# Kernel optimization log

Measured on AMD Instinct MI355X. Metric: run time of the kernel, lower is better.

## Reference

```python
import jax, jax.numpy as jnp
import numpy as np

D_MODEL = 1024
NUM_HEADS = 16


def setup_inputs() -> dict:
    key = jax.random.key(0)
    ks = jax.random.split(key, 5)
    B, S, D = 2, 2048, D_MODEL
    scale = 1.0 / np.sqrt(D)
    return {
        "x": jax.random.normal(ks[0], (B, S, D), dtype=jnp.float32),
        "q_proj_weight": jax.random.normal(ks[1], (D, D), dtype=jnp.float32) * scale,
        "k_proj_weight": jax.random.normal(ks[2], (D, D), dtype=jnp.float32) * scale,
        "v_proj_weight": jax.random.normal(ks[3], (D, D), dtype=jnp.float32) * scale,
        "o_proj_weight": jax.random.normal(ks[4], (D, D), dtype=jnp.float32) * scale,
    }


def _attn(x, qw, kw, vw, ow, num_heads):
    B, S, D = x.shape
    d_k = D // num_heads
    q = x @ qw.T  # [B,S,D]
    k = x @ kw.T
    v = x @ vw.T
    # split heads: [B, H, S, d_k]
    q = q.reshape(B, S, num_heads, d_k).transpose(0, 2, 1, 3)
    k = k.reshape(B, S, num_heads, d_k).transpose(0, 2, 1, 3)
    v = v.reshape(B, S, num_heads, d_k).transpose(0, 2, 1, 3)
    scores = jnp.einsum('bhqd,bhkd->bhqk', q, k) / jnp.sqrt(jnp.asarray(d_k, x.dtype))
    causal = jnp.tril(jnp.ones((S, S), dtype=bool))  # [S,S]
    scores = jnp.where(causal[None, None], scores, jnp.asarray(-jnp.inf, x.dtype))
    attn = jax.nn.softmax(scores, axis=-1)
    out = jnp.einsum('bhqk,bhkd->bhqd', attn, v)  # [B,H,S,d_k]
    out = out.transpose(0, 2, 1, 3).reshape(B, S, D)
    return out @ ow.T


def reference(x, q_proj_weight, k_proj_weight, v_proj_weight, o_proj_weight):
    return _attn(x, q_proj_weight, k_proj_weight, v_proj_weight, o_proj_weight, NUM_HEADS)
```

## Files before the change

kernel.cpp:

```cpp
#include <hip/hip_runtime.h>

typedef __attribute__((ext_vector_type(8))) short short8;
typedef __attribute__((ext_vector_type(4))) float f32x4;

#define MFMA(a,b,c) __builtin_amdgcn_mfma_f32_16x16x32_bf16((a),(b),(c),0,0,0)

#define B_  2
#define S_  2048
#define D_  1024
#define H_  16
#define DK  64
#define KDIM 1024

typedef unsigned int u32;
typedef __attribute__((address_space(1))) const u32 gu32;
typedef __attribute__((address_space(3))) u32 lu32;

__device__ __forceinline__ void gll16(const unsigned short* g, unsigned short* l){
  __builtin_amdgcn_global_load_lds((gu32*)g, (lu32*)l, 16, 0, 0);
}

__device__ __forceinline__ unsigned short f2bf(float f){
  unsigned int u = __float_as_uint(f);
  u += 0x7fffu + ((u >> 16) & 1u);
  return (unsigned short)(u >> 16);
}

__device__ __forceinline__ u32 pkbf(float lo, float hi){
  u32 a = __float_as_uint(lo) + 0x8000u;
  u32 b = __float_as_uint(hi) + 0x8000u;
  return __builtin_amdgcn_perm(b, a, 0x07060302u);
}

__global__ void cvt_all(const float* __restrict__ x,  const float* __restrict__ qw,
                        const float* __restrict__ kw, const float* __restrict__ vw,
                        const float* __restrict__ ow,
                        unsigned short* __restrict__ xb,  unsigned short* __restrict__ wqb,
                        unsigned short* __restrict__ wkb, unsigned short* __restrict__ wvb,
                        unsigned short* __restrict__ wob,
                        int n4x, int n4w){
  int i = blockIdx.x * 256 + threadIdx.x;
  const float* src; unsigned short* dst; int n4;
  switch (blockIdx.y) {
    case 0:  src = x;  dst = xb;  n4 = n4x; break;
    case 1:  src = qw; dst = wqb; n4 = n4w; break;
    case 2:  src = kw; dst = wkb; n4 = n4w; break;
    case 3:  src = vw; dst = wvb; n4 = n4w; break;
    default: src = ow; dst = wob; n4 = n4w; break;
  }
  if (i >= n4) return;
  float4 f = reinterpret_cast<const float4*>(src)[i];
  ushort4 u;
  u.x = f2bf(f.x); u.y = f2bf(f.y); u.z = f2bf(f.z); u.w = f2bf(f.w);
  reinterpret_cast<ushort4*>(dst)[i] = u;
}

struct Frags { short8 a0[4], a1[4], b0[2], b1[2]; };

__global__ __launch_bounds__(256) void gemm_qkv(
    const unsigned short* __restrict__ X,
    const unsigned short* __restrict__ Wq,
    const unsigned short* __restrict__ Wk,
    const unsigned short* __restrict__ Wv,
    unsigned short* __restrict__ Qo,
    unsigned short* __restrict__ Ko,
    unsigned short* __restrict__ Vo)
{
  const int z = blockIdx.z;
  const unsigned short* __restrict__ W = (z == 0) ? Wq : (z == 1) ? Wk : Wv;
  const int n0 = blockIdx.x * 64;
  const int m0 = blockIdx.y * 128;

  __shared__ unsigned short As[2][128 * 64];
  __shared__ unsigned short Bs[2][64 * 64];

  const int tid  = threadIdx.x;
  const int wid  = tid >> 6, lane = tid & 63;
  const int wm   = (wid >> 1) * 64, wn = (wid & 1) * 32;
  const int lr   = lane & 15, c = lane >> 4;
  const int sw   = lr & 7;
  const int pc0  = (c ^ sw) * 8;
  const int pc1  = ((c ^ 4) ^ sw) * 8;

  const int srow = lane >> 3;
  const int scol = ((lane & 7) ^ srow) * 8;
  const unsigned short* gA = X + (size_t)(m0 + wid * 32 + srow) * KDIM + scol;
  const unsigned short* gB = W + (size_t)(n0 + wid * 16 + srow) * KDIM + scol;

  auto stage = [&](int buf, int k0) {
    unsigned short* la = &As[buf][(wid * 32) * 64];
    unsigned short* lb = &Bs[buf][(wid * 16) * 64];
#pragma unroll
    for (int i = 0; i < 4; i++) gll16(gA + (size_t)(i * 8) * KDIM + k0, la + i * 512);
#pragma unroll
    for (int i = 0; i < 2; i++) gll16(gB + (size_t)(i * 8) * KDIM + k0, lb + i * 512);
  };

  auto ldfr = [&](int buf, Frags& f) {
    const unsigned short* AS = As[buf];
    const unsigned short* BS = Bs[buf];
#pragma unroll
    for (int i = 0; i < 4; i++) {
      f.a0[i] = *(const short8*)&AS[(wm + i * 16 + lr) * 64 + pc0];
      f.a1[i] = *(const short8*)&AS[(wm + i * 16 + lr) * 64 + pc1];
    }
#pragma unroll
    for (int j = 0; j < 2; j++) {
      f.b0[j] = *(const short8*)&BS[(wn + j * 16 + lr) * 64 + pc0];
      f.b1[j] = *(const short8*)&BS[(wn + j * 16 + lr) * 64 + pc1];
    }
  };

  f32x4 acc[4][2];
  const f32x4 z4 = {0.f, 0.f, 0.f, 0.f};
  for (int i = 0; i < 4; i++)
    for (int j = 0; j < 2; j++) acc[i][j] = z4;

  auto mfmas = [&](const Frags& f) {
    if (z == 2) {
#pragma unroll
      for (int i = 0; i < 4; i++)
#pragma unroll
        for (int j = 0; j < 2; j++) {
          acc[i][j] = MFMA(f.b0[j], f.a0[i], acc[i][j]);
          acc[i][j] = MFMA(f.b1[j], f.a1[i], acc[i][j]);
        }
    } else {
#pragma unroll
      for (int i = 0; i < 4; i++)
#pragma unroll
        for (int j = 0; j < 2; j++) {
          acc[i][j] = MFMA(f.a0[i], f.b0[j], acc[i][j]);
          acc[i][j] = MFMA(f.a1[i], f.b1[j], acc[i][j]);
        }
    }
  };

  stage(0, 0);
  stage(1, 64);

  Frags f;
  const int NT = KDIM / 64;
  for (int t = 0; t < NT - 2; ++t) {
    const int buf = t & 1;
    asm volatile("s_waitcnt vmcnt(6)" ::: "memory");
    __builtin_amdgcn_s_barrier();
    asm volatile("" ::: "memory");
    ldfr(buf, f);
    asm volatile("s_waitcnt lgkmcnt(0)" ::: "memory");
    __builtin_amdgcn_sched_barrier(0);
    __builtin_amdgcn_s_barrier();
    asm volatile("" ::: "memory");
    stage(buf, (t + 2) * 64);
    __builtin_amdgcn_sched_barrier(0);
    mfmas(f);
  }
  asm volatile("s_waitcnt vmcnt(6)" ::: "memory");
  __builtin_amdgcn_s_barrier();
  asm volatile("" ::: "memory");
  ldfr((NT - 2) & 1, f);
  mfmas(f);
  asm volatile("s_waitcnt vmcnt(0)" ::: "memory");
  __builtin_amdgcn_s_barrier();
  asm volatile("" ::: "memory");
  ldfr((NT - 1) & 1, f);
  mfmas(f);

  const int rbase = (lane >> 4) * 4;
  if (z == 2) {
    for (int i = 0; i < 4; i++)
      for (int j = 0; j < 2; j++)
        for (int r = 0; r < 4; r++) {
          int dfull = n0 + wn + j * 16 + rbase + r;
          int sfull = m0 + wm + i * 16 + lr;
          int h = dfull >> 6, d = dfull & 63;
          int bb = sfull >> 11, s = sfull & 2047;
          Vo[(((bb * H_ + h) * DK) + d) * S_ + s] = f2bf(acc[i][j][r]);
        }
  } else {
    for (int i = 0; i < 4; i++)
      for (int j = 0; j < 2; j++)
        for (int r = 0; r < 4; r++) {
          int m = m0 + wm + i * 16 + rbase + r;
          int n = n0 + wn + j * 16 + lr;
          float v = acc[i][j][r];
          int bb = m >> 11, s = m & 2047, h = n >> 6, d = n & 63;
          if (z == 0) {
            v *= 0.18033688f;
            Qo[(((bb * H_ + h) * S_) + s) * DK + d] = f2bf(v);
          } else {
            Ko[(((bb * H_ + h) * S_) + s) * DK + d] = f2bf(v);
          }
        }
  }
}

__global__ __launch_bounds__(512, 4) void attn(
    const unsigned short* __restrict__ Q,
    const unsigned short* __restrict__ K,
    const unsigned short* __restrict__ V,
    unsigned short* __restrict__ O)
{
  const int h = blockIdx.y, b = blockIdx.z;
  const int qt = b ? (15 - blockIdx.x) : blockIdx.x;

  const unsigned short* __restrict__ Qh = Q + (size_t)((b * H_ + h) * S_) * DK;
  const unsigned short* __restrict__ Kh = K + (size_t)((b * H_ + h) * S_) * DK;
  const unsigned short* __restrict__ Vh = V + (size_t)((b * H_ + h) * DK) * S_;

  __shared__ unsigned short Ks0[64 * 64];
  __shared__ unsigned short Ks1[64 * 64];
  __shared__ unsigned short Vs0[64 * 64];
  __shared__ unsigned short Vs1[64 * 64];
  __shared__ unsigned short Ps[8][16][72];

  const int tid = threadIdx.x, wid = tid >> 6, lane = tid & 63;
  const int lr = lane & 15;
  const int row4 = (lane >> 4) * 4;
  const int q0 = qt * 128;
  const int qcol = q0 + wid * 16 + lr;
  const int qwmin = q0 + wid * 16;
  const int qwmax = qwmin + 15;
  const int lk = (lane >> 4) * 8;

  const int pc0 = (((lane >> 4) + lr) & 7) * 8;
  const int pc1 = (((lane >> 4) + 4 + lr) & 7) * 8;

  const int sr8 = lane >> 3;
  const int sc8 = lane & 7;
  const int sg  = (sc8 - sr8) & 7;
  const int stRow = wid * 8 + sr8;
  const unsigned short* gK = Kh + (size_t)stRow * DK + sg * 8;
  const unsigned short* gV = Vh + (size_t)stRow * S_ + sg * 8;
  unsigned short* lK0 = &Ks0[wid * 8 * 64];
  unsigned short* lK1 = &Ks1[wid * 8 * 64];
  unsigned short* lV0 = &Vs0[wid * 8 * 64];
  unsigned short* lV1 = &Vs1[wid * 8 * 64];

  const short ONE = (short)0x3F80;
  const short8 ones = {ONE, ONE, ONE, ONE, ONE, ONE, ONE, ONE};

  short8 qf[2];
  qf[0] = *(const short8*)&Qh[(q0 + wid * 16 + lr) * DK + lk];
  qf[1] = *(const short8*)&Qh[(q0 + wid * 16 + lr) * DK + 32 + lk];

  const f32x4 z4 = {0.f, 0.f, 0.f, 0.f};
  f32x4 o[4];
  for (int i = 0; i < 4; i++) o[i] = z4;
  f32x4 rs = z4;

  auto tile = [&](int k0, const unsigned short* KS, const unsigned short* VS){
    if (k0 > qwmax) return;
    f32x4 sc[4];
    for (int nt = 0; nt < 4; nt++) {
      short8 kb0 = *(const short8*)&KS[(nt * 16 + lr) * 64 + pc0];
      short8 kb1 = *(const short8*)&KS[(nt * 16 + lr) * 64 + pc1];
      f32x4 s = MFMA(kb0, qf[0], z4);
      sc[nt] = MFMA(kb1, qf[1], s);
    }
    if (k0 + 63 > qwmin) {
      for (int nt = 0; nt < 4; nt++) {
        int kg = k0 + nt * 16 + row4;
        for (int r = 0; r < 4; r++)
          if (kg + r > qcol) sc[nt][r] = -INFINITY;
      }
    }
    for (int nt = 0; nt < 4; nt++) {
      float p0 = __builtin_amdgcn_exp2f(sc[nt][0]);
      float p1 = __builtin_amdgcn_exp2f(sc[nt][1]);
      float p2 = __builtin_amdgcn_exp2f(sc[nt][2]);
      float p3 = __builtin_amdgcn_exp2f(sc[nt][3]);
      uint2 pk;
      pk.x = pkbf(p0, p1);
      pk.y = pkbf(p2, p3);
      *(uint2*)&Ps[wid][lr][nt * 16 + row4] = pk;
    }
    short8 pf0 = *(const short8*)&Ps[wid][lr][lk];
    short8 pf1 = *(const short8*)&Ps[wid][lr][32 + lk];
    rs = MFMA(ones, pf0, rs);
    rs = MFMA(ones, pf1, rs);
    for (int dt = 0; dt < 4; dt++) {
      short8 vb0 = *(const short8*)&VS[(dt * 16 + lr) * 64 + pc0];
      short8 vb1 = *(const short8*)&VS[(dt * 16 + lr) * 64 + pc1];
      o[dt] = MFMA(vb0, pf0, o[dt]);
      o[dt] = MFMA(vb1, pf1, o[dt]);
    }
  };

  const int kt_end = 2 * qt + 2;

  gll16(gK, lK0);
  gll16(gV, lV0);

  for (int kt = 0; kt < kt_end; kt += 2) {
    const int k0 = kt * 64;
    __syncthreads();
    {
      gll16(gK + (size_t)(k0 + 64) * DK, lK1);
      gll16(gV + (k0 + 64),              lV1);
    }
    tile(k0, Ks0, Vs0);
    __syncthreads();
    if (kt + 2 < kt_end) {
      gll16(gK + (size_t)(k0 + 128) * DK, lK0);
      gll16(gV + (k0 + 128),              lV0);
    }
    tile(k0 + 64, Ks1, Vs1);
  }

  const float inv = 1.0f / rs[0];

  const int srow = q0 + wid * 16 + lr;
  for (int dt = 0; dt < 4; dt++) {
    uint2 pk;
    pk.x = pkbf(o[dt][0] * inv, o[dt][1] * inv);
    pk.y = pkbf(o[dt][2] * inv, o[dt][3] * inv);
    *(uint2*)&O[(size_t)(b * S_ + srow) * D_ + h * DK + dt * 16 + row4] = pk;
  }
}

__global__ __launch_bounds__(256) void gemm_oproj(
    const unsigned short* __restrict__ A,
    const unsigned short* __restrict__ W,
    float* __restrict__ out)
{
  const int n0 = blockIdx.x * 64;
  const int m0 = blockIdx.y * 128;

  __shared__ unsigned short As[2][128 * 64];
  __shared__ unsigned short Bs[2][64 * 64];

  const int tid  = threadIdx.x;
  const int wid  = tid >> 6, lane = tid & 63;
  const int wm   = (wid >> 1) * 64, wn = (wid & 1) * 32;
  const int lr   = lane & 15, c = lane >> 4;
  const int sw   = lr & 7;
  const int pc0  = (c ^ sw) * 8;
  const int pc1  = ((c ^ 4) ^ sw) * 8;

  const int srow = lane >> 3;
  const int scol = ((lane & 7) ^ srow) * 8;
  const unsigned short* gA = A + (size_t)(m0 + wid * 32 + srow) * KDIM + scol;
  const unsigned short* gB = W + (size_t)(n0 + wid * 16 + srow) * KDIM + scol;

  auto stage = [&](int buf, int k0) {
    unsigned short* la = &As[buf][(wid * 32) * 64];
    unsigned short* lb = &Bs[buf][(wid * 16) * 64];
#pragma unroll
    for (int i = 0; i < 4; i++) gll16(gA + (size_t)(i * 8) * KDIM + k0, la + i * 512);
#pragma unroll
    for (int i = 0; i < 2; i++) gll16(gB + (size_t)(i * 8) * KDIM + k0, lb + i * 512);
  };

  auto ldfr = [&](int buf, Frags& f) {
    const unsigned short* AS = As[buf];
    const unsigned short* BS = Bs[buf];
#pragma unroll
    for (int i = 0; i < 4; i++) {
      f.a0[i] = *(const short8*)&AS[(wm + i * 16 + lr) * 64 + pc0];
      f.a1[i] = *(const short8*)&AS[(wm + i * 16 + lr) * 64 + pc1];
    }
#pragma unroll
    for (int j = 0; j < 2; j++) {
      f.b0[j] = *(const short8*)&BS[(wn + j * 16 + lr) * 64 + pc0];
      f.b1[j] = *(const short8*)&BS[(wn + j * 16 + lr) * 64 + pc1];
    }
  };

  f32x4 acc[4][2];
  const f32x4 z4 = {0.f, 0.f, 0.f, 0.f};
  for (int i = 0; i < 4; i++)
    for (int j = 0; j < 2; j++) acc[i][j] = z4;

  auto mfmas = [&](const Frags& f) {
#pragma unroll
    for (int i = 0; i < 4; i++)
#pragma unroll
      for (int j = 0; j < 2; j++) {
        acc[i][j] = MFMA(f.a0[i], f.b0[j], acc[i][j]);
        acc[i][j] = MFMA(f.a1[i], f.b1[j], acc[i][j]);
      }
  };

  stage(0, 0);
  stage(1, 64);

  Frags f;
  const int NT = KDIM / 64;
  for (int t = 0; t < NT - 2; ++t) {
    const int buf = t & 1;
    asm volatile("s_waitcnt vmcnt(6)" ::: "memory");
    __builtin_amdgcn_s_barrier();
    asm volatile("" ::: "memory");
    ldfr(buf, f);
    asm volatile("s_waitcnt lgkmcnt(0)" ::: "memory");
    __builtin_amdgcn_sched_barrier(0);
    __builtin_amdgcn_s_barrier();
    asm volatile("" ::: "memory");
    stage(buf, (t + 2) * 64);
    __builtin_amdgcn_sched_barrier(0);
    mfmas(f);
  }
  asm volatile("s_waitcnt vmcnt(6)" ::: "memory");
  __builtin_amdgcn_s_barrier();
  asm volatile("" ::: "memory");
  ldfr((NT - 2) & 1, f);
  mfmas(f);
  asm volatile("s_waitcnt vmcnt(0)" ::: "memory");
  __builtin_amdgcn_s_barrier();
  asm volatile("" ::: "memory");
  ldfr((NT - 1) & 1, f);
  mfmas(f);

  const int rbase = (lane >> 4) * 4;
  for (int i = 0; i < 4; i++)
    for (int j = 0; j < 2; j++)
      for (int r = 0; r < 4; r++) {
        int m = m0 + wm + i * 16 + rbase + r;
        int n = n0 + wn + j * 16 + lr;
        out[(size_t)m * D_ + n] = acc[i][j][r];
      }
}

extern "C" void kernel_launch(void* const* d_in, const int* in_sizes, int n_in,
                              void* d_out, int out_size, void* d_ws, size_t ws_size,
                              hipStream_t stream) {
  const float* x  = (const float*)d_in[0];
  const float* qw = (const float*)d_in[1];
  const float* kw = (const float*)d_in[2];
  const float* vw = (const float*)d_in[3];
  const float* ow = (const float*)d_in[4];
  float* out = (float*)d_out;

  char* ws = (char*)d_ws;
  size_t off = 0;
  auto alloc = [&](size_t bytes) -> void* {
    void* p = ws + off;
    off += (bytes + 255) & ~(size_t)255;
    return p;
  };
  const size_t XN = (size_t)B_ * S_ * D_;
  const size_t WN = (size_t)D_ * D_;
  unsigned short* xb  = (unsigned short*)alloc(XN * 2);
  unsigned short* wqb = (unsigned short*)alloc(WN * 2);
  unsigned short* wkb = (unsigned short*)alloc(WN * 2);
  unsigned short* wvb = (unsigned short*)alloc(WN * 2);
  unsigned short* wob = (unsigned short*)alloc(WN * 2);
  unsigned short* Qb  = (unsigned short*)alloc(XN * 2);
  unsigned short* Kb  = (unsigned short*)alloc(XN * 2);
  unsigned short* Vb  = (unsigned short*)alloc(XN * 2);
  unsigned short* Ob  = (unsigned short*)alloc(XN * 2);

  cvt_all<<<dim3((XN / 4 + 255) / 256, 5), dim3(256), 0, stream>>>(
      x, qw, kw, vw, ow, xb, wqb, wkb, wvb, wob, (int)(XN / 4), (int)(WN / 4));

  gemm_qkv<<<dim3(D_ / 64, (B_ * S_) / 128, 3), dim3(256), 0, stream>>>(
      xb, wqb, wkb, wvb, Qb, Kb, Vb);

  attn<<<dim3(S_ / 128, H_, B_), dim3(512), 0, stream>>>(Qb, Kb, Vb, Ob);

  gemm_oproj<<<dim3(D_ / 64, (B_ * S_) / 128), dim3(256), 0, stream>>>(Ob, wob, out);
}
```

Baseline: 162.8 us.

## Fuse Q/K/V projections into one GEMM block sharing the X tile

Measured after the change: 152.6 us. -6.3%, faster.

```diff
diff --git a/kernel.cpp b/kernel.cpp
--- a/kernel.cpp
+++ b/kernel.cpp
@@ -55,9 +55,9 @@
   reinterpret_cast<ushort4*>(dst)[i] = u;
 }
 
-struct Frags { short8 a0[4], a1[4], b0[2], b1[2]; };
-
-__global__ __launch_bounds__(256) void gemm_qkv(
+struct FragsQKV { short8 a0[4], a1[4], b0[3][2], b1[3][2]; };
+
+__global__ __launch_bounds__(256, 2) void gemm_qkv(
     const unsigned short* __restrict__ X,
     const unsigned short* __restrict__ Wq,
     const unsigned short* __restrict__ Wk,
@@ -66,13 +66,11 @@
     unsigned short* __restrict__ Ko,
     unsigned short* __restrict__ Vo)
 {
-  const int z = blockIdx.z;
-  const unsigned short* __restrict__ W = (z == 0) ? Wq : (z == 1) ? Wk : Wv;
   const int n0 = blockIdx.x * 64;
   const int m0 = blockIdx.y * 128;
 
   __shared__ unsigned short As[2][128 * 64];
-  __shared__ unsigned short Bs[2][64 * 64];
+  __shared__ unsigned short Bs[2][3][64 * 64];
 
   const int tid  = threadIdx.x;
   const int wid  = tid >> 6, lane = tid & 63;
@@ -84,7 +82,278 @@
 
   const int srow = lane >> 3;
   const int scol = ((lane & 7) ^ srow) * 8;
-  const unsigned short* gA = X + (size_t)(m0 + wid * 32 + srow) * KDIM + scol;
+  const unsigned short* gA  = X  + (size_t)(m0 + wid * 32 + srow) * KDIM + scol;
+  const unsigned short* gBq = Wq + (size_t)(n0 + wid * 16 + srow) * KDIM + scol;
+  const unsigned short* gBk = Wk + (size_t)(n0 + wid * 16 + srow) * KDIM + scol;
+  const unsigned short* gBv = Wv + (size_t)(n0 + wid * 16 + srow) * KDIM + scol;
+
+  auto stage = [&](int buf, int k0) {
+    unsigned short* la  = &As[buf][(wid * 32) * 64];
+    unsigned short* lbq = &Bs[buf][0][(wid * 16) * 64];
+    unsigned short* lbk = &Bs[buf][1][(wid * 16) * 64];
+    unsigned short* lbv = &Bs[buf][2][(wid * 16) * 64];
+#pragma unroll
+    for (int i = 0; i < 4; i++) gll16(gA + (size_t)(i * 8) * KDIM + k0, la + i * 512);
+#pragma unroll
+    for (int i = 0; i < 2; i++) gll16(gBq + (size_t)(i * 8) * KDIM + k0, lbq + i * 512);
+#pragma unroll
+    for (int i = 0; i < 2; i++) gll16(gBk + (size_t)(i * 8) * KDIM + k0, lbk + i * 512);
+#pragma unroll
+    for (int i = 0; i < 2; i++) gll16(gBv + (size_t)(i * 8) * KDIM + k0, lbv + i * 512);
+  };
+
+  auto ldfr = [&](int buf, FragsQKV& f) {
+    const unsigned short* AS = As[buf];
+#pragma unroll
+    for (int i = 0; i < 4; i++) {
+      f.a0[i] = *(const short8*)&AS[(wm + i * 16 + lr) * 64 + pc0];
+      f.a1[i] = *(const short8*)&AS[(wm + i * 16 + lr) * 64 + pc1];
+    }
+#pragma unroll
+    for (int z = 0; z < 3; z++) {
+      const unsigned short* BS = Bs[buf][z];
+#pragma unroll
+      for (int j = 0; j < 2; j++) {
+        f.b0[z][j] = *(const short8*)&BS[(wn + j * 16 + lr) * 64 + pc0];
+        f.b1[z][j] = *(const short8*)&BS[(wn + j * 16 + lr) * 64 + pc1];
+      }
+    }
+  };
+
+  f32x4 acc[3][4][2];
+  const f32x4 z4 = {0.f, 0.f, 0.f, 0.f};
+#pragma unroll
+  for (int z = 0; z < 3; z++)
+    for (int i = 0; i < 4; i++)
+      for (int j = 0; j < 2; j++) acc[z][i][j] = z4;
+
+  auto mfmas = [&](const FragsQKV& f) {
+#pragma unroll
+    for (int z = 0; z < 3; z++) {
+      if (z == 2) {
+#pragma unroll
+        for (int i = 0; i < 4; i++)
+#pragma unroll
+          for (int j = 0; j < 2; j++) {
+            acc[z][i][j] = MFMA(f.b0[z][j], f.a0[i], acc[z][i][j]);
+            acc[z][i][j] = MFMA(f.b1[z][j], f.a1[i], acc[z][i][j]);
+          }
+      } else {
+#pragma unroll
+        for (int i = 0; i < 4; i++)
+#pragma unroll
+          for (int j = 0; j < 2; j++) {
+            acc[z][i][j] = MFMA(f.a0[i], f.b0[z][j], acc[z][i][j]);
+            acc[z][i][j] = MFMA(f.a1[i], f.b1[z][j], acc[z][i][j]);
+          }
+      }
+    }
+  };
+
+  stage(0, 0);
+  stage(1, 64);
+
+  FragsQKV f;
+  const int NT = KDIM / 64;
+  for (int t = 0; t < NT - 2; ++t) {
+    const int buf = t & 1;
+    asm volatile("s_waitcnt vmcnt(10)" ::: "memory");
+    __builtin_amdgcn_s_barrier();
+    asm volatile("" ::: "memory");
+    ldfr(buf, f);
+    asm volatile("s_waitcnt lgkmcnt(0)" ::: "memory");
+    __builtin_amdgcn_sched_barrier(0);
+    __builtin_amdgcn_s_barrier();
+    asm volatile("" ::: "memory");
+    stage(buf, (t + 2) * 64);
+    __builtin_amdgcn_sched_barrier(0);
+    mfmas(f);
+  }
+  asm volatile("s_waitcnt vmcnt(10)" ::: "memory");
+  __builtin_amdgcn_s_barrier();
+  asm volatile("" ::: "memory");
+  ldfr((NT - 2) & 1, f);
+  mfmas(f);
+  asm volatile("s_waitcnt vmcnt(0)" ::: "memory");
+  __builtin_amdgcn_s_barrier();
+  asm volatile("" ::: "memory");
+  ldfr((NT - 1) & 1, f);
+  mfmas(f);
+
+  const int rbase = (lane >> 4) * 4;
+  for (int i = 0; i < 4; i++)
+    for (int j = 0; j < 2; j++)
+      for (int r = 0; r < 4; r++) {
+        int m = m0 + wm + i * 16 + rbase + r;
+        int n = n0 + wn + j * 16 + lr;
+        int bb = m >> 11, s = m & 2047, h = n >> 6, d = n & 63;
+        float vq = acc[0][i][j][r] * 0.18033688f;
+        Qo[(((bb * H_ + h) * S_) + s) * DK + d] = f2bf(vq);
+        Ko[(((bb * H_ + h) * S_) + s) * DK + d] = f2bf(acc[1][i][j][r]);
+      }
+  for (int i = 0; i < 4; i++)
+    for (int j = 0; j < 2; j++)
+      for (int r = 0; r < 4; r++) {
+        int dfull = n0 + wn + j * 16 + rbase + r;
+        int sfull = m0 + wm + i * 16 + lr;
+        int h = dfull >> 6, d = dfull & 63;
+        int bb = sfull >> 11, s = sfull & 2047;
+        Vo[(((bb * H_ + h) * DK) + d) * S_ + s] = f2bf(acc[2][i][j][r]);
+      }
+}
+
+__global__ __launch_bounds__(512, 4) void attn(
+    const unsigned short* __restrict__ Q,
+    const unsigned short* __restrict__ K,
+    const unsigned short* __restrict__ V,
+    unsigned short* __restrict__ O)
+{
+  const int h = blockIdx.y, b = blockIdx.z;
+  const int qt = b ? (15 - blockIdx.x) : blockIdx.x;
+
+  const unsigned short* __restrict__ Qh = Q + (size_t)((b * H_ + h) * S_) * DK;
+  const unsigned short* __restrict__ Kh = K + (size_t)((b * H_ + h) * S_) * DK;
+  const unsigned short* __restrict__ Vh = V + (size_t)((b * H_ + h) * DK) * S_;
+
+  __shared__ unsigned short Ks0[64 * 64];
+  __shared__ unsigned short Ks1[64 * 64];
+  __shared__ unsigned short Vs0[64 * 64];
+  __shared__ unsigned short Vs1[64 * 64];
+  __shared__ unsigned short Ps[8][16][72];
+
+  const int tid = threadIdx.x, wid = tid >> 6, lane = tid & 63;
+  const int lr = lane & 15;
+  const int row4 = (lane >> 4) * 4;
+  const int q0 = qt * 128;
+  const int qcol = q0 + wid * 16 + lr;
+  const int qwmin = q0 + wid * 16;
+  const int qwmax = qwmin + 15;
+  const int lk = (lane >> 4) * 8;
+
+  const int pc0 = (((lane >> 4) + lr) & 7) * 8;
+  const int pc1 = (((lane >> 4) + 4 + lr) & 7) * 8;
+
+  const int sr8 = lane >> 3;
+  const int sc8 = lane & 7;
+  const int sg  = (sc8 - sr8) & 7;
+  const int stRow = wid * 8 + sr8;
+  const unsigned short* gK = Kh + (size_t)stRow * DK + sg * 8;
+  const unsigned short* gV = Vh + (size_t)stRow * S_ + sg * 8;
+  unsigned short* lK0 = &Ks0[wid * 8 * 64];
+  unsigned short* lK1 = &Ks1[wid * 8 * 64];
+  unsigned short* lV0 = &Vs0[wid * 8 * 64];
+  unsigned short* lV1 = &Vs1[wid * 8 * 64];
+
+  const short ONE = (short)0x3F80;
+  const short8 ones = {ONE, ONE, ONE, ONE, ONE, ONE, ONE, ONE};
+
+  short8 qf[2];
+  qf[0] = *(const short8*)&Qh[(q0 + wid * 16 + lr) * DK + lk];
+  qf[1] = *(const short8*)&Qh[(q0 + wid * 16 + lr) * DK + 32 + lk];
+
+  const f32x4 z4 = {0.f, 0.f, 0.f, 0.f};
+  f32x4 o[4];
+  for (int i = 0; i < 4; i++) o[i] = z4;
+  f32x4 rs = z4;
+
+  auto tile = [&](int k0, const unsigned short* KS, const unsigned short* VS){
+    if (k0 > qwmax) return;
+    f32x4 sc[4];
+    __builtin_amdgcn_s_setprio(1);
+    for (int nt = 0; nt < 4; nt++) {
+      short8 kb0 = *(const short8*)&KS[(nt * 16 + lr) * 64 + pc0];
+      short8 kb1 = *(const short8*)&KS[(nt * 16 + lr) * 64 + pc1];
+      f32x4 s = MFMA(kb0, qf[0], z4);
+      sc[nt] = MFMA(kb1, qf[1], s);
+    }
+    __builtin_amdgcn_s_setprio(0);
+    if (k0 + 63 > qwmin) {
+      for (int nt = 0; nt < 4; nt++) {
+        int kg = k0 + nt * 16 + row4;
+        for (int r = 0; r < 4; r++)
+          if (kg + r > qcol) sc[nt][r] = -INFINITY;
+      }
+    }
+    for (int nt = 0; nt < 4; nt++) {
+      float p0 = __builtin_amdgcn_exp2f(sc[nt][0]);
+      float p1 = __builtin_amdgcn_exp2f(sc[nt][1]);
+      float p2 = __builtin_amdgcn_exp2f(sc[nt][2]);
+      float p3 = __builtin_amdgcn_exp2f(sc[nt][3]);
+      uint2 pk;
+      pk.x = pkbf(p0, p1);
+      pk.y = pkbf(p2, p3);
+      *(uint2*)&Ps[wid][lr][nt * 16 + row4] = pk;
+    }
+    short8 pf0 = *(const short8*)&Ps[wid][lr][lk];
+    short8 pf1 = *(const short8*)&Ps[wid][lr][32 + lk];
+    __builtin_amdgcn_s_setprio(1);
+    rs = MFMA(ones, pf0, rs);
+    rs = MFMA(ones, pf1, rs);
+    for (int dt = 0; dt < 4; dt++) {
+      short8 vb0 = *(const short8*)&VS[(dt * 16 + lr) * 64 + pc0];
+      short8 vb1 = *(const short8*)&VS[(dt * 16 + lr) * 64 + pc1];
+      o[dt] = MFMA(vb0, pf0, o[dt]);
+      o[dt] = MFMA(vb1, pf1, o[dt]);
+    }
+    __builtin_amdgcn_s_setprio(0);
+  };
+
+  const int kt_end = 2 * qt + 2;
+
+  gll16(gK, lK0);
+  gll16(gV, lV0);
+
+  for (int kt = 0; kt < kt_end; kt += 2) {
+    const int k0 = kt * 64;
+    __syncthreads();
+    {
+      gll16(gK + (size_t)(k0 + 64) * DK, lK1);
+      gll16(gV + (k0 + 64),              lV1);
+    }
+    tile(k0, Ks0, Vs0);
+    __syncthreads();
+    if (kt + 2 < kt_end) {
+      gll16(gK + (size_t)(k0 + 128) * DK, lK0);
+      gll16(gV + (k0 + 128),              lV0);
+    }
+    tile(k0 + 64, Ks1, Vs1);
+  }
+
+  const float inv = 1.0f / rs[0];
+
+  const int srow = q0 + wid * 16 + lr;
+  for (int dt = 0; dt < 4; dt++) {
+    uint2 pk;
+    pk.x = pkbf(o[dt][0] * inv, o[dt][1] * inv);
+    pk.y = pkbf(o[dt][2] * inv, o[dt][3] * inv);
+    *(uint2*)&O[(size_t)(b * S_ + srow) * D_ + h * DK + dt * 16 + row4] = pk;
+  }
+}
+
+struct Frags { short8 a0[4], a1[4], b0[2], b1[2]; };
+
+__global__ __launch_bounds__(256) void gemm_oproj(
+    const unsigned short* __restrict__ A,
+    const unsigned short* __restrict__ W,
+    float* __restrict__ out)
+{
+  const int n0 = blockIdx.x * 64;
+  const int m0 = blockIdx.y * 128;
+
+  __shared__ unsigned short As[2][128 * 64];
+  __shared__ unsigned short Bs[2][64 * 64];
+
+  const int tid  = threadIdx.x;
+  const int wid  = tid >> 6, lane = tid & 63;
+  const int wm   = (wid >> 1) * 64, wn = (wid & 1) * 32;
+  const int lr   = lane & 15, c = lane >> 4;
+  const int sw   = lr & 7;
+  const int pc0  = (c ^ sw) * 8;
+  const int pc1  = ((c ^ 4) ^ sw) * 8;
+
+  const int srow = lane >> 3;
+  const int scol = ((lane & 7) ^ srow) * 8;
+  const unsigned short* gA = A + (size_t)(m0 + wid * 32 + srow) * KDIM + scol;
   const unsigned short* gB = W + (size_t)(n0 + wid * 16 + srow) * KDIM + scol;
 
   auto stage = [&](int buf, int k0) {
@@ -117,23 +386,13 @@
     for (int j = 0; j < 2; j++) acc[i][j] = z4;
 
   auto mfmas = [&](const Frags& f) {
-    if (z == 2) {
-#pragma unroll
-      for (int i = 0; i < 4; i++)
-#pragma unroll
-        for (int j = 0; j < 2; j++) {
-          acc[i][j] = MFMA(f.b0[j], f.a0[i], acc[i][j]);
-          acc[i][j] = MFMA(f.b1[j], f.a1[i], acc[i][j]);
-        }
-    } else {
-#pragma unroll
-      for (int i = 0; i < 4; i++)
-#pragma unroll
-        for (int j = 0; j < 2; j++) {
-          acc[i][j] = MFMA(f.a0[i], f.b0[j], acc[i][j]);
-          acc[i][j] = MFMA(f.a1[i], f.b1[j], acc[i][j]);
-        }
-    }
+#pragma unroll
+    for (int i = 0; i < 4; i++)
+#pragma unroll
+      for (int j = 0; j < 2; j++) {
+        acc[i][j] = MFMA(f.a0[i], f.b0[j], acc[i][j]);
+        acc[i][j] = MFMA(f.a1[i], f.b1[j], acc[i][j]);
+      }
   };
 
   stage(0, 0);
@@ -167,252 +426,6 @@
   mfmas(f);
 
   const int rbase = (lane >> 4) * 4;
-  if (z == 2) {
-    for (int i = 0; i < 4; i++)
-      for (int j = 0; j < 2; j++)
-        for (int r = 0; r < 4; r++) {
-          int dfull = n0 + wn + j * 16 + rbase + r;
-          int sfull = m0 + wm + i * 16 + lr;
-          int h = dfull >> 6, d = dfull & 63;
-          int bb = sfull >> 11, s = sfull & 2047;
-          Vo[(((bb * H_ + h) * DK) + d) * S_ + s] = f2bf(acc[i][j][r]);
-        }
-  } else {
-    for (int i = 0; i < 4; i++)
-      for (int j = 0; j < 2; j++)
-        for (int r = 0; r < 4; r++) {
-          int m = m0 + wm + i * 16 + rbase + r;
-          int n = n0 + wn + j * 16 + lr;
-          float v = acc[i][j][r];
-          int bb = m >> 11, s = m & 2047, h = n >> 6, d = n & 63;
-          if (z == 0) {
-            v *= 0.18033688f;
-            Qo[(((bb * H_ + h) * S_) + s) * DK + d] = f2bf(v);
-          } else {
-            Ko[(((bb * H_ + h) * S_) + s) * DK + d] = f2bf(v);
-          }
-        }
-  }
-}
-
-__global__ __launch_bounds__(512, 4) void attn(
-    const unsigned short* __restrict__ Q,
-    const unsigned short* __restrict__ K,
-    const unsigned short* __restrict__ V,
-    unsigned short* __restrict__ O)
-{
-  const int h = blockIdx.y, b = blockIdx.z;
-  const int qt = b ? (15 - blockIdx.x) : blockIdx.x;
-
-  const unsigned short* __restrict__ Qh = Q + (size_t)((b * H_ + h) * S_) * DK;
-  const unsigned short* __restrict__ Kh = K + (size_t)((b * H_ + h) * S_) * DK;
-  const unsigned short* __restrict__ Vh = V + (size_t)((b * H_ + h) * DK) * S_;
-
-  __shared__ unsigned short Ks0[64 * 64];
-  __shared__ unsigned short Ks1[64 * 64];
-  __shared__ unsigned short Vs0[64 * 64];
-  __shared__ unsigned short Vs1[64 * 64];
-  __shared__ unsigned short Ps[8][16][72];
-
-  const int tid = threadIdx.x, wid = tid >> 6, lane = tid & 63;
-  const int lr = lane & 15;
-  const int row4 = (lane >> 4) * 4;
-  const int q0 = qt * 128;
-  const int qcol = q0 + wid * 16 + lr;
-  const int qwmin = q0 + wid * 16;
-  const int qwmax = qwmin + 15;
-  const int lk = (lane >> 4) * 8;
-
-  const int pc0 = (((lane >> 4) + lr) & 7) * 8;
-  const int pc1 = (((lane >> 4) + 4 + lr) & 7) * 8;
-
-  const int sr8 = lane >> 3;
-  const int sc8 = lane & 7;
-  const int sg  = (sc8 - sr8) & 7;
-  const int stRow = wid * 8 + sr8;
-  const unsigned short* gK = Kh + (size_t)stRow * DK + sg * 8;
-  const unsigned short* gV = Vh + (size_t)stRow * S_ + sg * 8;
-  unsigned short* lK0 = &Ks0[wid * 8 * 64];
-  unsigned short* lK1 = &Ks1[wid * 8 * 64];
-  unsigned short* lV0 = &Vs0[wid * 8 * 64];
-  unsigned short* lV1 = &Vs1[wid * 8 * 64];
-
-  const short ONE = (short)0x3F80;
-  const short8 ones = {ONE, ONE, ONE, ONE, ONE, ONE, ONE, ONE};
-
-  short8 qf[2];
-  qf[0] = *(const short8*)&Qh[(q0 + wid * 16 + lr) * DK + lk];
-  qf[1] = *(const short8*)&Qh[(q0 + wid * 16 + lr) * DK + 32 + lk];
-
-  const f32x4 z4 = {0.f, 0.f, 0.f, 0.f};
-  f32x4 o[4];
-  for (int i = 0; i < 4; i++) o[i] = z4;
-  f32x4 rs = z4;
-
-  auto tile = [&](int k0, const unsigned short* KS, const unsigned short* VS){
-    if (k0 > qwmax) return;
-    f32x4 sc[4];
-    for (int nt = 0; nt < 4; nt++) {
-      short8 kb0 = *(const short8*)&KS[(nt * 16 + lr) * 64 + pc0];
-      short8 kb1 = *(const short8*)&KS[(nt * 16 + lr) * 64 + pc1];
-      f32x4 s = MFMA(kb0, qf[0], z4);
-      sc[nt] = MFMA(kb1, qf[1], s);
-    }
-    if (k0 + 63 > qwmin) {
-      for (int nt = 0; nt < 4; nt++) {
-        int kg = k0 + nt * 16 + row4;
-        for (int r = 0; r < 4; r++)
-          if (kg + r > qcol) sc[nt][r] = -INFINITY;
-      }
-    }
-    for (int nt = 0; nt < 4; nt++) {
-      float p0 = __builtin_amdgcn_exp2f(sc[nt][0]);
-      float p1 = __builtin_amdgcn_exp2f(sc[nt][1]);
-      float p2 = __builtin_amdgcn_exp2f(sc[nt][2]);
-      float p3 = __builtin_amdgcn_exp2f(sc[nt][3]);
-      uint2 pk;
-      pk.x = pkbf(p0, p1);
-      pk.y = pkbf(p2, p3);
-      *(uint2*)&Ps[wid][lr][nt * 16 + row4] = pk;
-    }
-    short8 pf0 = *(const short8*)&Ps[wid][lr][lk];
-    short8 pf1 = *(const short8*)&Ps[wid][lr][32 + lk];
-    rs = MFMA(ones, pf0, rs);
-    rs = MFMA(ones, pf1, rs);
-    for (int dt = 0; dt < 4; dt++) {
-      short8 vb0 = *(const short8*)&VS[(dt * 16 + lr) * 64 + pc0];
-      short8 vb1 = *(const short8*)&VS[(dt * 16 + lr) * 64 + pc1];
-      o[dt] = MFMA(vb0, pf0, o[dt]);
-      o[dt] = MFMA(vb1, pf1, o[dt]);
-    }
-  };
-
-  const int kt_end = 2 * qt + 2;
-
-  gll16(gK, lK0);
-  gll16(gV, lV0);
-
-  for (int kt = 0; kt < kt_end; kt += 2) {
-    const int k0 = kt * 64;
-    __syncthreads();
-    {
-      gll16(gK + (size_t)(k0 + 64) * DK, lK1);
-      gll16(gV + (k0 + 64),              lV1);
-    }
-    tile(k0, Ks0, Vs0);
-    __syncthreads();
-    if (kt + 2 < kt_end) {
-      gll16(gK + (size_t)(k0 + 128) * DK, lK0);
-      gll16(gV + (k0 + 128),              lV0);
-    }
-    tile(k0 + 64, Ks1, Vs1);
-  }
-
-  const float inv = 1.0f / rs[0];
-
-  const int srow = q0 + wid * 16 + lr;
-  for (int dt = 0; dt < 4; dt++) {
-    uint2 pk;
-    pk.x = pkbf(o[dt][0] * inv, o[dt][1] * inv);
-    pk.y = pkbf(o[dt][2] * inv, o[dt][3] * inv);
-    *(uint2*)&O[(size_t)(b * S_ + srow) * D_ + h * DK + dt * 16 + row4] = pk;
-  }
-}
-
-__global__ __launch_bounds__(256) void gemm_oproj(
-    const unsigned short* __restrict__ A,
-    const unsigned short* __restrict__ W,
-    float* __restrict__ out)
-{
-  const int n0 = blockIdx.x * 64;
-  const int m0 = blockIdx.y * 128;
-
-  __shared__ unsigned short As[2][128 * 64];
-  __shared__ unsigned short Bs[2][64 * 64];
-
-  const int tid  = threadIdx.x;
-  const int wid  = tid >> 6, lane = tid & 63;
-  const int wm   = (wid >> 1) * 64, wn = (wid & 1) * 32;
-  const int lr   = lane & 15, c = lane >> 4;
-  const int sw   = lr & 7;
-  const int pc0  = (c ^ sw) * 8;
-  const int pc1  = ((c ^ 4) ^ sw) * 8;
-
-  const int srow = lane >> 3;
-  const int scol = ((lane & 7) ^ srow) * 8;
-  const unsigned short* gA = A + (size_t)(m0 + wid * 32 + srow) * KDIM + scol;
-  const unsigned short* gB = W + (size_t)(n0 + wid * 16 + srow) * KDIM + scol;
-
-  auto stage = [&](int buf, int k0) {
-    unsigned short* la = &As[buf][(wid * 32) * 64];
-    unsigned short* lb = &Bs[buf][(wid * 16) * 64];
-#pragma unroll
-    for (int i = 0; i < 4; i++) gll16(gA + (size_t)(i * 8) * KDIM + k0, la + i * 512);
-#pragma unroll
-    for (int i = 0; i < 2; i++) gll16(gB + (size_t)(i * 8) * KDIM + k0, lb + i * 512);
-  };
-
-  auto ldfr = [&](int buf, Frags& f) {
-    const unsigned short* AS = As[buf];
-    const unsigned short* BS = Bs[buf];
-#pragma unroll
-    for (int i = 0; i < 4; i++) {
-      f.a0[i] = *(const short8*)&AS[(wm + i * 16 + lr) * 64 + pc0];
-      f.a1[i] = *(const short8*)&AS[(wm + i * 16 + lr) * 64 + pc1];
-    }
-#pragma unroll
-    for (int j = 0; j < 2; j++) {
-      f.b0[j] = *(const short8*)&BS[(wn + j * 16 + lr) * 64 + pc0];
-      f.b1[j] = *(const short8*)&BS[(wn + j * 16 + lr) * 64 + pc1];
-    }
-  };
-
-  f32x4 acc[4][2];
-  const f32x4 z4 = {0.f, 0.f, 0.f, 0.f};
-  for (int i = 0; i < 4; i++)
-    for (int j = 0; j < 2; j++) acc[i][j] = z4;
-
-  auto mfmas = [&](const Frags& f) {
-#pragma unroll
-    for (int i = 0; i < 4; i++)
-#pragma unroll
-      for (int j = 0; j < 2; j++) {
-        acc[i][j] = MFMA(f.a0[i], f.b0[j], acc[i][j]);
-        acc[i][j] = MFMA(f.a1[i], f.b1[j], acc[i][j]);
-      }
-  };
-
-  stage(0, 0);
-  stage(1, 64);
-
-  Frags f;
-  const int NT = KDIM / 64;
-  for (int t = 0; t < NT - 2; ++t) {
-    const int buf = t & 1;
-    asm volatile("s_waitcnt vmcnt(6)" ::: "memory");
-    __builtin_amdgcn_s_barrier();
-    asm volatile("" ::: "memory");
-    ldfr(buf, f);
-    asm volatile("s_waitcnt lgkmcnt(0)" ::: "memory");
-    __builtin_amdgcn_sched_barrier(0);
-    __builtin_amdgcn_s_barrier();
-    asm volatile("" ::: "memory");
-    stage(buf, (t + 2) * 64);
-    __builtin_amdgcn_sched_barrier(0);
-    mfmas(f);
-  }
-  asm volatile("s_waitcnt vmcnt(6)" ::: "memory");
-  __builtin_amdgcn_s_barrier();
-  asm volatile("" ::: "memory");
-  ldfr((NT - 2) & 1, f);
-  mfmas(f);
-  asm volatile("s_waitcnt vmcnt(0)" ::: "memory");
-  __builtin_amdgcn_s_barrier();
-  asm volatile("" ::: "memory");
-  ldfr((NT - 1) & 1, f);
-  mfmas(f);
-
-  const int rbase = (lane >> 4) * 4;
   for (int i = 0; i < 4; i++)
     for (int j = 0; j < 2; j++)
       for (int r = 0; r < 4; r++) {
@@ -454,7 +467,7 @@
   cvt_all<<<dim3((XN / 4 + 255) / 256, 5), dim3(256), 0, stream>>>(
       x, qw, kw, vw, ow, xb, wqb, wkb, wvb, wob, (int)(XN / 4), (int)(WN / 4));
 
-  gemm_qkv<<<dim3(D_ / 64, (B_ * S_) / 128, 3), dim3(256), 0, stream>>>(
+  gemm_qkv<<<dim3(D_ / 64, (B_ * S_) / 128), dim3(256), 0, stream>>>(
       xb, wqb, wkb, wvb, Qb, Kb, Vb);
 
   attn<<<dim3(S_ / 128, H_, B_), dim3(512), 0, stream>>>(Qb, Kb, Vb, Ob);
```
